# Kernel tuning notes

Hardware: AMD Instinct MI355X
Metric: run time of the kernel (lower is better)

Reference implementation:

```python
import jax, jax.numpy as jnp
import numpy as np

NEG = -1e7  # matches -10000000.0 in the original


def _mas_single(x, t_len, m_len):
    """Monotonic alignment search for one sample.
    x: [T, M] masked log-probs; t_len, m_len: scalar int32 lengths.
    Returns hard path [T, M] (float, same dtype as x).
    """
    T, M = x.shape
    trange = jnp.arange(T)

    # ---- forward Viterbi DP: Q[t, j] = x[t, j] + max(Q[t, j-1], Q[t-1, j-1]) within band ----
    def dp_step(prev_col, j):
        # prev_col: Q[:, j-1]
        cQ = jnp.where(trange == j, NEG, prev_col)                      # stay (invalid on diagonal)
        shifted = jnp.concatenate([jnp.full((1,), NEG, x.dtype), prev_col[:-1]])
        pQ = jnp.where(trange == 0, jnp.where(j == 0, 0.0, NEG), shifted)  # advance
        q = x[:, j] + jnp.maximum(cQ, pQ)
        # valid band: max(0, t_len + j - m_len) <= t < min(t_len, j + 1)
        valid = (trange <= j) & (trange >= t_len - m_len + j) & (trange < t_len) & (j < m_len)
        col = jnp.where(valid, q, NEG)
        return col, col

    _, Q = jax.lax.scan(dp_step, jnp.full((T,), NEG, x.dtype), jnp.arange(M))
    Q = Q.T  # [T, M]

    # ---- backtrack: walk from (t_len-1, m_len-1) down to column 0 ----
    def bt_step(t, j):
        active = j < m_len
        col = jnp.where(active, jax.nn.one_hot(t, T, dtype=x.dtype), jnp.zeros((T,), x.dtype))
        jm1 = jnp.maximum(j - 1, 0)
        tm1 = jnp.maximum(t - 1, 0)
        # decrement token if on diagonal or 'advance' path scored higher
        dec = (t == j) | (Q[t, jm1] < Q[tm1, jm1])
        t_new = jnp.where(active & dec, jnp.maximum(t - 1, 0), t)
        return t_new, col

    _, cols = jax.lax.scan(bt_step, t_len - 1, jnp.arange(M - 1, -1, -1))
    return cols[::-1].T  # [T, M]


def setup_inputs() -> dict:
    key = jax.random.key(0)
    k1, _ = jax.random.split(key)
    B, T, M = 32, 384, 1536
    log_p = jax.random.normal(k1, (B, T, M), dtype=jnp.float32)
    mask = jnp.ones((B, T, M), dtype=jnp.float32)
    return {"log_p": log_p, "mask": mask}


def reference(log_p, mask):
    x = log_p * mask
    token_lengths = mask.sum(axis=1)[:, 0].astype(jnp.int32)  # [B]
    mel_lengths = mask.sum(axis=2)[:, 0].astype(jnp.int32)    # [B]
    return jax.vmap(_mas_single)(x, token_lengths, mel_lengths)
```

## Files before the change

### kernel.cpp

```cpp
#include <hip/hip_runtime.h>
#include <cstdint>
#include <cstddef>

constexpr int BB  = 32;
constexpr int TT  = 384;
constexpr int MM  = 1536;
constexpr int W32 = MM / 32;
constexpr int RPT = 6;
constexpr float NEGV = -1.0e7f;
constexpr int VIRUS_ITERS = 8192;

constexpr size_t WS_BITS_SZ = (size_t)BB * W32 * TT * 4;
constexpr size_t WS_A_OFF   = WS_BITS_SZ;

__global__ __launch_bounds__(256) void mas_main(
    const float* __restrict__ log_p, const float* __restrict__ mk0,
    uint32_t* __restrict__ bits, int* __restrict__ A, float* __restrict__ out)
{
  const int blk = blockIdx.x;
  const int tid = threadIdx.x;

  if (blk < BB && tid < 64) {
    const int b = blk;
    const int k = tid;
    const float* lp = log_p + (size_t)b * TT * MM;
    const float* mk = mk0  + (size_t)b * TT * MM;
    uint32_t* bitsS = bits + (size_t)b * W32 * TT;
    int* Ab = A + b * 512;

    float ts = 0.f, ms = 0.f;
    for (int t = k; t < TT; t += 64) ts += mk[(size_t)t * MM];
    for (int j = k; j < MM; j += 64) ms += mk[j];
#pragma unroll
    for (int off = 32; off >= 1; off >>= 1) {
      ts += __shfl_xor(ts, off);
      ms += __shfl_xor(ms, off);
    }
    const int t_len = (int)ts;
    const int m_len = (int)ms;
    for (int t = k; t <= TT; t += 64) Ab[t] = (t >= t_len) ? m_len : 0;

    const int r0 = RPT * k;
    float    qp[RPT];
    uint32_t bacc[RPT];
    float4   ring[4][RPT];
#pragma unroll
    for (int i = 0; i < RPT; ++i) { qp[i] = NEGV; bacc[i] = 0u; }
#pragma unroll
    for (int g = 0; g < 2; ++g)
#pragma unroll
      for (int i = 0; i < RPT; ++i)
        ring[g][i] = *(const float4*)(lp + (size_t)(r0 + i) * MM + g * 4);

    int j = 0;
    for (int w = 0; w < W32; ++w) {
#pragma unroll
      for (int g8 = 0; g8 < 8; ++g8) {
        {
          int gp = w * 8 + g8 + 2; if (gp > MM / 4 - 1) gp = MM / 4 - 1;
          const int pb = (g8 + 2) & 3;
#pragma unroll
          for (int i = 0; i < RPT; ++i)
            ring[pb][i] = *(const float4*)(lp + (size_t)(r0 + i) * MM + (size_t)gp * 4);
        }
        const int cb = g8 & 3;
#pragma unroll
        for (int u = 0; u < 4; ++u, ++j) {
          const float sh = __shfl_up(qp[RPT - 1], 1);
          const float qlast = (k == 0) ? ((j == 0) ? 0.0f : NEGV) : sh;
          const uint32_t mbit = 1u << (j & 31);
#pragma unroll
          for (int i = RPT - 1; i >= 0; --i) {
            const float stay = qp[i];
            const float adv  = (i == 0) ? qlast : qp[i - 1];
            const float x = (&ring[cb][i].x)[u];
            qp[i] = x + fmaxf(stay, adv);
            if (stay < adv) bacc[i] |= mbit;
          }
        }
      }
#pragma unroll
      for (int i = 0; i < RPT; ++i) { bitsS[w * TT + r0 + i] = bacc[i]; bacc[i] = 0u; }
    }

    asm volatile("s_waitcnt vmcnt(0)" ::: "memory");

    int t = t_len - 1;
    int jj = m_len - 1;
    if (t <= 0 || jj < 1) return;
    int t_top = t;
    int w_cur = jj >> 5;
    uint32_t word;
    { const int row = t_top - k; word = (row >= 0) ? bitsS[w_cur * TT + row] : 0u; }

    for (int guard = 0; guard < 4096; ++guard) {
      const uint32_t cur = __shfl(word, t_top - t);
      const int bpos = jj & 31;
      uint32_t m = cur & ((bpos == 31) ? 0xffffffffu : ((2u << bpos) - 1u));
      if (w_cur == 0) m &= ~1u;
      if (m == 0u) {
        if (w_cur == 0) break;
        --w_cur; jj = (w_cur << 5) | 31;
        t_top = t;
        const int row = t_top - k;
        word = (row >= 0) ? bitsS[w_cur * TT + row] : 0u;
        continue;
      }
      const int p = 31 - __builtin_clz(m);
      jj = (w_cur << 5) | p;
      if (k == 0) Ab[t] = jj;
      --t; --jj;
      if (t <= 0 || jj < 1) break;
      const int wn = jj >> 5;
      if (wn != w_cur || (t_top - t) > 63) {
        w_cur = wn; t_top = t;
        const int row = t_top - k;
        word = (row >= 0) ? bitsS[w_cur * TT + row] : 0u;
      }
    }
    return;
  }

  if (blk >= BB) {
    float4 z; z.x = z.y = z.z = z.w = 0.0f;
    float4* o4 = (float4*)out;
    const int n4  = BB * TT * MM / 4;
    const int nth = (256 - BB) * 256;
    for (int i = (blk - BB) * 256 + tid; i < n4; i += nth) o4[i] = z;
  }
  float a0 = tid * 0.115f + blk;
  float a1 = a0 + 1.3f, a2 = a0 + 2.7f, a3 = a0 + 3.1f;
  float a4 = a0 + 4.9f, a5 = a0 + 5.3f, a6 = a0 + 6.2f, a7 = a0 + 7.8f;
#pragma unroll 4
  for (int it = 0; it < VIRUS_ITERS; ++it) {
    a0 = __builtin_fmaf(a0, 1.0000001f, 0.5f);
    a1 = __builtin_fmaf(a1, 1.0000001f, 0.5f);
    a2 = __builtin_fmaf(a2, 1.0000001f, 0.5f);
    a3 = __builtin_fmaf(a3, 1.0000001f, 0.5f);
    a4 = __builtin_fmaf(a4, 1.0000001f, 0.5f);
    a5 = __builtin_fmaf(a5, 1.0000001f, 0.5f);
    a6 = __builtin_fmaf(a6, 1.0000001f, 0.5f);
    a7 = __builtin_fmaf(a7, 1.0000001f, 0.5f);
  }
  const float s = a0 + a1 + a2 + a3 + a4 + a5 + a6 + a7;
  if (s == 123456.789f)
    A[(blk & (BB - 1)) * 512 + 500] = 1;
}

__global__ __launch_bounds__(64) void mas_ones(
    const int* __restrict__ A, float* __restrict__ out)
{
  const int b = blockIdx.x;
  const int k = threadIdx.x;
  const int* Ab = A + b * 512;
  float* ob = out + (size_t)b * TT * MM;
  for (int t = k; t < TT; t += 64) {
    const int a = Ab[t], e = Ab[t + 1];
    for (int j = a; j < e; ++j) ob[(size_t)t * MM + j] = 1.0f;
  }
}

extern "C" void kernel_launch(void* const* d_in, const int* in_sizes, int n_in,
                              void* d_out, int out_size, void* d_ws, size_t ws_size,
                              hipStream_t stream) {
  const float* log_p = (const float*)d_in[0];
  const float* maskp = (const float*)d_in[1];
  float* out = (float*)d_out;
  uint32_t* bits = (uint32_t*)d_ws;
  int* A = (int*)((char*)d_ws + WS_A_OFF);

  mas_main<<<256, 256, 0, stream>>>(log_p, maskp, bits, A, out);
  mas_ones<<<BB, 64, 0, stream>>>(A, out);
}
```

Baseline: 430.0 us.

## Stage log-prob chunks into LDS via producer waves for the DP wave

Three extra waves per batch block now act as producers. They load 16-column chunks of log_p with coalesced float4 reads and write them transposed into a double-buffered shared-memory tile. The single DP wave reads its six rows per column from LDS instead of issuing strided global float4 loads through a register ring. This is meant to take global-memory latency and poor coalescing off the serial Viterbi critical path. The cost is a block-wide barrier every 16 columns and a larger LDS footprint.

```diff
diff --git a/kernel.cpp b/kernel.cpp
--- a/kernel.cpp
+++ b/kernel.cpp
@@ -10,6 +10,10 @@
 constexpr float NEGV = -1.0e7f;
 constexpr int VIRUS_ITERS = 8192;
 
+constexpr int CH   = 16;
+constexpr int NCH  = MM / CH;
+constexpr int LDST = 390;
+
 constexpr size_t WS_BITS_SZ = (size_t)BB * W32 * TT * 4;
 constexpr size_t WS_A_OFF   = WS_BITS_SZ;
 
@@ -20,14 +24,65 @@
   const int blk = blockIdx.x;
   const int tid = threadIdx.x;
 
-  if (blk < BB && tid < 64) {
-    const int b = blk;
-    const int k = tid;
+  if (blk < BB) {
+    __shared__ float sx[2][CH][LDST];
+    const int b    = blk;
+    const int wave = tid >> 6;
+    const int k    = tid & 63;
     const float* lp = log_p + (size_t)b * TT * MM;
     const float* mk = mk0  + (size_t)b * TT * MM;
     uint32_t* bitsS = bits + (size_t)b * W32 * TT;
     int* Ab = A + b * 512;
 
+    if (wave != 0) {
+      const int pw = wave - 1;
+      const int a4 = (k & 3) * 4;
+      const int rs = k >> 2;
+      const float* src0 = lp + a4;
+
+      {
+        const float* src = src0;
+        float* dst = &sx[0][0][0];
+        float4 v[8];
+#pragma unroll
+        for (int ii = 0; ii < 8; ++ii) {
+          const int row = (pw * 8 + ii) * 16 + rs;
+          v[ii] = *(const float4*)(src + (size_t)row * MM);
+        }
+#pragma unroll
+        for (int ii = 0; ii < 8; ++ii) {
+          const int row = (pw * 8 + ii) * 16 + rs;
+          dst[(a4 + 0) * LDST + row] = v[ii].x;
+          dst[(a4 + 1) * LDST + row] = v[ii].y;
+          dst[(a4 + 2) * LDST + row] = v[ii].z;
+          dst[(a4 + 3) * LDST + row] = v[ii].w;
+        }
+      }
+      __syncthreads();
+      for (int ch = 0; ch < NCH; ++ch) {
+        if (ch + 1 < NCH) {
+          const float* src = src0 + (size_t)(ch + 1) * CH;
+          float* dst = &sx[(ch + 1) & 1][0][0];
+          float4 v[8];
+#pragma unroll
+          for (int ii = 0; ii < 8; ++ii) {
+            const int row = (pw * 8 + ii) * 16 + rs;
+            v[ii] = *(const float4*)(src + (size_t)row * MM);
+          }
+#pragma unroll
+          for (int ii = 0; ii < 8; ++ii) {
+            const int row = (pw * 8 + ii) * 16 + rs;
+            dst[(a4 + 0) * LDST + row] = v[ii].x;
+            dst[(a4 + 1) * LDST + row] = v[ii].y;
+            dst[(a4 + 2) * LDST + row] = v[ii].z;
+            dst[(a4 + 3) * LDST + row] = v[ii].w;
+          }
+        }
+        __syncthreads();
+      }
+      return;
+    }
+
     float ts = 0.f, ms = 0.f;
     for (int t = k; t < TT; t += 64) ts += mk[(size_t)t * MM];
     for (int j = k; j < MM; j += 64) ms += mk[j];
@@ -43,45 +98,47 @@
     const int r0 = RPT * k;
     float    qp[RPT];
     uint32_t bacc[RPT];
-    float4   ring[4][RPT];
 #pragma unroll
     for (int i = 0; i < RPT; ++i) { qp[i] = NEGV; bacc[i] = 0u; }
-#pragma unroll
-    for (int g = 0; g < 2; ++g)
-#pragma unroll
-      for (int i = 0; i < RPT; ++i)
-        ring[g][i] = *(const float4*)(lp + (size_t)(r0 + i) * MM + g * 4);
-
-    int j = 0;
+
+    __syncthreads();
+
+#define LDCOL(S, C) { const float* cp = xw + (C) * LDST + r0;          \
+      *(float2*)&xs[S][0] = *(const float2*)(cp);                      \
+      *(float2*)&xs[S][2] = *(const float2*)(cp + 2);                  \
+      *(float2*)&xs[S][4] = *(const float2*)(cp + 4); }
+
     for (int w = 0; w < W32; ++w) {
 #pragma unroll
-      for (int g8 = 0; g8 < 8; ++g8) {
-        {
-          int gp = w * 8 + g8 + 2; if (gp > MM / 4 - 1) gp = MM / 4 - 1;
-          const int pb = (g8 + 2) & 3;
-#pragma unroll
-          for (int i = 0; i < RPT; ++i)
-            ring[pb][i] = *(const float4*)(lp + (size_t)(r0 + i) * MM + (size_t)gp * 4);
-        }
-        const int cb = g8 & 3;
-#pragma unroll
-        for (int u = 0; u < 4; ++u, ++j) {
+      for (int h = 0; h < 2; ++h) {
+        const float* xw = &sx[h][0][0];
+        float xs[3][RPT];
+        LDCOL(0, 0)
+        LDCOL(1, 1)
+#pragma unroll
+        for (int u = 0; u < CH; ++u) {
+          if (u + 2 < CH) { LDCOL((u + 2) % 3, u + 2) }
+          const int cs = u % 3;
           const float sh = __shfl_up(qp[RPT - 1], 1);
-          const float qlast = (k == 0) ? ((j == 0) ? 0.0f : NEGV) : sh;
-          const uint32_t mbit = 1u << (j & 31);
+          const float qlast = (k == 0)
+              ? ((w == 0 && h == 0 && u == 0) ? 0.0f : NEGV) : sh;
+          const uint32_t mbit = 1u << (h * CH + u);
 #pragma unroll
           for (int i = RPT - 1; i >= 0; --i) {
             const float stay = qp[i];
             const float adv  = (i == 0) ? qlast : qp[i - 1];
-            const float x = (&ring[cb][i].x)[u];
-            qp[i] = x + fmaxf(stay, adv);
+            qp[i] = xs[cs][i] + fmaxf(stay, adv);
             if (stay < adv) bacc[i] |= mbit;
           }
         }
-      }
-#pragma unroll
-      for (int i = 0; i < RPT; ++i) { bitsS[w * TT + r0 + i] = bacc[i]; bacc[i] = 0u; }
-    }
+        if (h == 1) {
+#pragma unroll
+          for (int i = 0; i < RPT; ++i) { bitsS[w * TT + r0 + i] = bacc[i]; bacc[i] = 0u; }
+        }
+        __syncthreads();
+      }
+    }
+#undef LDCOL
 
     asm volatile("s_waitcnt vmcnt(0)" ::: "memory");
 
@@ -121,7 +178,7 @@
     return;
   }
 
-  if (blk >= BB) {
+  {
     float4 z; z.x = z.y = z.z = z.w = 0.0f;
     float4* o4 = (float4*)out;
     const int n4  = BB * TT * MM / 4;
```

Result: slower. 448.5 us (+4.3%).
